# Kernel optimization log

Measured on AMD Instinct MI355X. Metric: run time of the kernel, lower is better.

## Reference

```python
import jax, jax.numpy as jnp
import numpy as np

# Dimensions
T = 1024      # tokens
D = 1024      # d_model
DFF = 1024    # expert intermediate dim
R = 64        # tucker rank (r_in == r_out)
G = 8         # n_group
E = 32        # experts_per_group
NEXP = G * E  # 256 routed experts
K = 8         # top-k


def setup_inputs() -> dict:
    key = jax.random.key(0)
    ks = jax.random.split(key, 12)
    s = 0.02
    return {
        "x": jax.random.normal(ks[0], (T, D), jnp.float32),
        "Wg": jax.random.normal(ks[1], (D, NEXP), jnp.float32) * s,
        "uin_gate": jax.random.normal(ks[2], (G, D, R), jnp.float32) * s,
        "core_gate": jax.random.normal(ks[3], (G, E, R, R), jnp.float32) * s,
        "uout_gate": jax.random.normal(ks[4], (G, R, DFF), jnp.float32) * s,
        "uin_up": jax.random.normal(ks[5], (G, D, R), jnp.float32) * s,
        "core_up": jax.random.normal(ks[6], (G, E, R, R), jnp.float32) * s,
        "uout_up": jax.random.normal(ks[7], (G, R, DFF), jnp.float32) * s,
        "uin_down": jax.random.normal(ks[8], (G, DFF, R), jnp.float32) * s,
        "core_down": jax.random.normal(ks[9], (G, E, R, R), jnp.float32) * s,
        "uout_down": jax.random.normal(ks[10], (G, R, D), jnp.float32) * s,
    }


def _moe_forward(x, Wg, uin_gate, core_gate, uout_gate,
                 uin_up, core_up, uout_up,
                 uin_down, core_down, uout_down):
    Tn, d = x.shape
    # Router: top-k over 256 experts, softmax over the k logits (fp32 as in torch)
    logits = x @ Wg                                   # [T, NEXP]
    w, sel = jax.lax.top_k(logits, K)                 # [T, K]
    w = jax.nn.softmax(w.astype(jnp.float32), axis=-1).astype(x.dtype)

    e = sel.reshape(-1)                               # [F] global expert id
    g = e // E                                        # [F] group id
    tok = jnp.repeat(jnp.arange(Tn), K)               # [F] source token id
    mask = (g[:, None] == jnp.arange(G)[None, :]).astype(x.dtype)  # [F, G]

    def gather_in(uin):
        # project tokens with every group's u_in once, then gather per pair
        pre = jnp.einsum('td,gdr->gtr', x, uin)       # [G, T, R]
        return pre[g, tok]                            # [F, R]

    def core_apply(xin, core):
        # per-pair Tucker core slice bmm: x.unsqueeze(1) @ core[rel_idx]
        slices = core.reshape(G * E, R, R)[e]         # [F, R, R] gather
        return jnp.einsum('fr,fro->fo', xin, slices)  # [F, R]

    def group_out(h, U):
        # per-pair group-specific projection: h[f] @ U[g_f]
        out = jnp.zeros((h.shape[0], U.shape[-1]), h.dtype)
        for gi in range(G):  # fixed small loop over 8 groups
            out = out + (h * mask[:, gi:gi + 1]) @ U[gi]
        return out

    gate_h = group_out(core_apply(gather_in(uin_gate), core_gate), uout_gate)  # [F, DFF]
    up_h = group_out(core_apply(gather_in(uin_up), core_up), uout_up)          # [F, DFF]
    act = jax.nn.silu(gate_h) * up_h                                           # SwiGLU
    xin_d = group_out(act, uin_down)                                           # [F, R]
    out_f = group_out(core_apply(xin_d, core_down), uout_down)                 # [F, D]
    out_f = out_f * w.reshape(-1)[:, None]
    # scatter-add expert outputs back to tokens
    return jax.ops.segment_sum(out_f, tok, num_segments=Tn)


def reference(x, Wg, uin_gate, core_gate, uout_gate,
              uin_up, core_up, uout_up,
              uin_down, core_down, uout_down):
    return _moe_forward(x, Wg, uin_gate, core_gate, uout_gate,
                        uin_up, core_up, uout_up,
                        uin_down, core_down, uout_down)
```

## Files before the change

### kernel.cpp

```cpp
#include <hip/hip_runtime.h>
#include <hip/hip_bf16.h>
#include <math.h>


#define T_ 1024
#define D_ 1024
#define DFF_ 1024
#define R_ 64
#define G_ 8
#define E_ 32
#define NEXP_ 256
#define K_ 8
#define F_ 8192
#define PKZ_ 2
#define DKZ_ 4
#define LP_ 72

typedef short bf16x8 __attribute__((ext_vector_type(8)));
typedef float f32x4 __attribute__((ext_vector_type(4)));

__device__ __forceinline__ unsigned short f2bf(float f) {
  unsigned int u = __float_as_uint(f);
  u += 0x7fffu + ((u >> 16) & 1u);
  return (unsigned short)(u >> 16);
}

__device__ __forceinline__ void stage_tile(short* dst, const unsigned short* src,
                                           int gp, int tid) {
  for (int idx = tid; idx < 512; idx += 256) {
    int r = idx >> 3, c8 = (idx & 7) << 3;
    *(uint4*)&dst[r * LP_ + c8] = *(const uint4*)&src[(size_t)r * gp + c8];
  }
}

__device__ __forceinline__ void stage_tile_guard(short* dst, const unsigned short* src,
                                                 int gp, int rows_valid, int tid) {
  for (int idx = tid; idx < 512; idx += 256) {
    int r = idx >> 3, c8 = (idx & 7) << 3;
    uint4 v = make_uint4(0u, 0u, 0u, 0u);
    if (r < rows_valid) v = *(const uint4*)&src[(size_t)r * gp + c8];
    *(uint4*)&dst[r * LP_ + c8] = v;
  }
}

__device__ __forceinline__ void stage_tile_f32(short* dst, const float* src,
                                               int gp, int tid) {
  for (int idx = tid; idx < 512; idx += 256) {
    int r = idx >> 3, c8 = (idx & 7) << 3;
    const float* s = &src[(size_t)r * gp + c8];
    float4 v0 = *(const float4*)s;
    float4 v1 = *(const float4*)(s + 4);
    uint4 u;
    u.x = ((unsigned)f2bf(v0.y) << 16) | f2bf(v0.x);
    u.y = ((unsigned)f2bf(v0.w) << 16) | f2bf(v0.z);
    u.z = ((unsigned)f2bf(v1.y) << 16) | f2bf(v1.x);
    u.w = ((unsigned)f2bf(v1.w) << 16) | f2bf(v1.z);
    *(uint4*)&dst[r * LP_ + c8] = u;
  }
}

__device__ __forceinline__ void mma_strip(const short* As, const short* Bs,
                                          int ms, int lane, f32x4* acc) {
  int lm = lane & 15;
  int lk = (lane >> 4) << 3;
#pragma unroll
  for (int kc = 0; kc < 64; kc += 32) {
    bf16x8 a = *(const bf16x8*)&As[(ms + lm) * LP_ + kc + lk];
#pragma unroll
    for (int nt = 0; nt < 4; ++nt) {
      bf16x8 b = *(const bf16x8*)&Bs[(nt * 16 + lm) * LP_ + kc + lk];
      acc[nt] = __builtin_amdgcn_mfma_f32_16x16x32_bf16(a, b, acc[nt], 0, 0, 0);
    }
  }
}

__global__ __launch_bounds__(256) void k_prep(
    const float* __restrict__ x,
    const float* __restrict__ s0, const float* __restrict__ s1,
    const float* __restrict__ s2, const float* __restrict__ s3,
    const float* __restrict__ s4, const float* __restrict__ s5,
    unsigned short* __restrict__ xb,
    unsigned short* __restrict__ d0, unsigned short* __restrict__ d1,
    unsigned short* __restrict__ d2, unsigned short* __restrict__ d3,
    unsigned short* __restrict__ d4, unsigned short* __restrict__ d5,
    int* __restrict__ cnt, int* __restrict__ tickets, float* __restrict__ Yf) {
  __shared__ float shbuf[64 * 65];
  int b = blockIdx.x;
  int id = b >> 7, rem = b & 127, g = rem >> 4, tile = rem & 15;
  if (id == 6) {
    size_t base = ((size_t)g * 16 + tile) * 8192;
    for (int i = threadIdx.x; i < 2048; i += 256) {
      size_t idx = base + (size_t)i * 4;
      float4 v = *(const float4*)&x[idx];
      xb[idx + 0] = f2bf(v.x);
      xb[idx + 1] = f2bf(v.y);
      xb[idx + 2] = f2bf(v.z);
      xb[idx + 3] = f2bf(v.w);
    }
    size_t ybase = ((size_t)g * 16 + tile) * 4096;
    float4 z4 = make_float4(0.f, 0.f, 0.f, 0.f);
    for (int i = threadIdx.x; i < 1024; i += 256)
      *(float4*)&Yf[ybase + (size_t)i * 4] = z4;
    if (g == 0 && tile == 0) {
      cnt[threadIdx.x] = 0;
      if (threadIdx.x == 0) tickets[0] = 0;
    }
    return;
  }
  const float* src = id == 0 ? s0 : id == 1 ? s1 : id == 2 ? s2 : id == 3 ? s3 : id == 4 ? s4 : s5;
  unsigned short* dst = id == 0 ? d0 : id == 1 ? d1 : id == 2 ? d2 : id == 3 ? d3 : id == 4 ? d4 : d5;
  if (id < 3) {
    int r0 = tile * 64;
    for (int idx = threadIdx.x; idx < 4096; idx += 256) {
      int r = idx >> 6, c = idx & 63;
      shbuf[r * 65 + c] = src[((size_t)g * 1024 + r0 + r) * 64 + c];
    }
    __syncthreads();
    for (int idx = threadIdx.x; idx < 4096; idx += 256) {
      int c = idx >> 6, r = idx & 63;
      dst[((size_t)g * 64 + c) * 1024 + r0 + r] = f2bf(shbuf[r * 65 + c]);
    }
  } else {
    int c0 = tile * 64;
    for (int idx = threadIdx.x; idx < 4096; idx += 256) {
      int r = idx >> 6, c = idx & 63;
      shbuf[r * 65 + c] = src[((size_t)g * 64 + r) * 1024 + c0 + c];
    }
    __syncthreads();
    if (id == 5) {
      for (int idx = threadIdx.x; idx < 4096; idx += 256) {
        int c = idx >> 6, r = idx & 63;
        dst[(size_t)(c0 + c) * 512 + g * 64 + r] = f2bf(shbuf[r * 65 + c]);
      }
    } else {
      for (int idx = threadIdx.x; idx < 4096; idx += 256) {
        int c = idx >> 6, r = idx & 63;
        dst[((size_t)g * 1024 + c0 + c) * 64 + r] = f2bf(shbuf[r * 65 + c]);
      }
    }
  }
}

__global__ __launch_bounds__(256) void k_pre_router(
    const float* __restrict__ x, const float* __restrict__ Wg,
    const unsigned short* __restrict__ xb,
    const unsigned short* __restrict__ uinT_g, const unsigned short* __restrict__ uinT_u,
    float* __restrict__ Pgp, float* __restrict__ Pup,
    float* __restrict__ wsm, int* __restrict__ bucket, int* __restrict__ cnt,
    int* __restrict__ tickets, int* __restrict__ off) {
  __shared__ float smf[8192];
  __shared__ int lastfl;
  int b = blockIdx.x;
  int tid = threadIdx.x;
  if (b >= 128) {
    int b2 = b - 128;
    int tile = b2 & 15, g = (b2 >> 4) & 7, zz = b2 >> 7;
    int gu = zz >> 1, kz = zz & 1;
    const unsigned short* U = gu ? uinT_u : uinT_g;
    float* P = gu ? Pup : Pgp;
    int t0 = tile * 64;
    short* As = (short*)smf;
    short* Bs = (short*)smf + 64 * LP_;
    int lane = tid & 63, ms = (tid >> 6) * 16;
    f32x4 acc[4] = {};
    int dlo = kz * (D_ / PKZ_);
    for (int dc = dlo; dc < dlo + D_ / PKZ_; dc += 64) {
      stage_tile(As, xb + (size_t)t0 * D_ + dc, D_, tid);
      stage_tile(Bs, U + (size_t)g * 64 * 1024 + dc, 1024, tid);
      __syncthreads();
      mma_strip(As, Bs, ms, lane, acc);
      __syncthreads();
    }
    int lm = lane & 15, lq = (lane >> 4) * 4;
#pragma unroll
    for (int nt = 0; nt < 4; ++nt)
#pragma unroll
      for (int r = 0; r < 4; ++r)
        P[((size_t)(kz * G_ + g) * T_ + t0 + ms + lq + r) * R_ + nt * 16 + lm] = acc[nt][r];
    return;
  }
  int t0 = b * 8;
  for (int i = tid; i < 2048; i += 256) {
    int j = i >> 8, d4 = (i & 255) << 2;
    *(float4*)&smf[j * 1024 + d4] = *(const float4*)&x[(size_t)(t0 + j) * D_ + d4];
  }
  __syncthreads();
  int e = tid;
  float a[8] = {};
#pragma unroll 2
  for (int d2 = 0; d2 < 1024; d2 += 4) {
    float w0 = Wg[(size_t)(d2 + 0) * NEXP_ + e];
    float w1 = Wg[(size_t)(d2 + 1) * NEXP_ + e];
    float w2 = Wg[(size_t)(d2 + 2) * NEXP_ + e];
    float w3 = Wg[(size_t)(d2 + 3) * NEXP_ + e];
#pragma unroll
    for (int j = 0; j < 8; ++j) {
      float4 xv = *(const float4*)&smf[j * 1024 + d2];
      float aj = a[j];
      aj = fmaf(xv.x, w0, aj);
      aj = fmaf(xv.y, w1, aj);
      aj = fmaf(xv.z, w2, aj);
      aj = fmaf(xv.w, w3, aj);
      a[j] = aj;
    }
  }
  __syncthreads();
  float* lg = smf;
#pragma unroll
  for (int j = 0; j < 8; ++j) lg[j * 256 + e] = a[j];
  __syncthreads();
  int wave = tid >> 6, lane = tid & 63;
  for (int kk = 0; kk < 2; ++kk) {
    int j = wave * 2 + kk;
    int t = t0 + j;
    float v[4];
    int idx[4];
#pragma unroll
    for (int j2 = 0; j2 < 4; ++j2) {
      idx[j2] = lane + 64 * j2;
      v[j2] = lg[j * 256 + idx[j2]];
    }
    float topv[K_];
    int topi[K_];
#pragma unroll
    for (int k = 0; k < K_; ++k) {
      float bv = v[0];
      int bi = idx[0];
#pragma unroll
      for (int j2 = 1; j2 < 4; ++j2)
        if (v[j2] > bv || (v[j2] == bv && idx[j2] < bi)) { bv = v[j2]; bi = idx[j2]; }
#pragma unroll
      for (int o2 = 32; o2 > 0; o2 >>= 1) {
        float ov = __shfl_xor(bv, o2);
        int oi = __shfl_xor(bi, o2);
        if (ov > bv || (ov == bv && oi < bi)) { bv = ov; bi = oi; }
      }
      topv[k] = bv;
      topi[k] = bi;
#pragma unroll
      for (int j2 = 0; j2 < 4; ++j2)
        if (idx[j2] == bi) v[j2] = -INFINITY;
    }
    float m = topv[0];
    float ev[K_];
    float s = 0.f;
#pragma unroll
    for (int k = 0; k < K_; ++k) { ev[k] = expf(topv[k] - m); s += ev[k]; }
    float inv = 1.f / s;
    if (lane < K_) {
      wsm[t * K_ + lane] = ev[lane] * inv;
      int r1 = atomicAdd(&cnt[topi[lane]], 1);
      bucket[topi[lane] * 1024 + r1] = t * K_ + lane;
    }
  }
  __threadfence();
  __syncthreads();
  if (tid == 0) lastfl = (atomicAdd(&tickets[0], 1) == 127) ? 1 : 0;
  __syncthreads();
  if (lastfl) {
    int* s = (int*)smf;
    int i = tid;
    int c0 = atomicAdd(&cnt[i], 0);
    s[i] = c0;
    __syncthreads();
    for (int d = 1; d < NEXP_; d <<= 1) {
      int vv = (i >= d) ? s[i - d] : 0;
      __syncthreads();
      s[i] += vv;
      __syncthreads();
    }
    off[i + 1] = s[i];
    if (i == 0) off[0] = 0;
  }
}

__global__ __launch_bounds__(256) void k_core_gu(const float* __restrict__ Pgp,
                                                 const float* __restrict__ Pup,
                                                 const float* __restrict__ core_g,
                                                 const float* __restrict__ core_u,
                                                 const int* __restrict__ bucket,
                                                 const int* __restrict__ off,
                                                 unsigned short* __restrict__ xgb,
                                                 unsigned short* __restrict__ xub) {
  int e = blockIdx.x >> 1, half = blockIdx.x & 1;
  int g = e >> 5;
  __shared__ float cg[4096], cu[4096];
  __shared__ float rg[4][64], ru[4][64];
  int tid = threadIdx.x;
  for (int i = tid; i < 1024; i += 256) {
    *(float4*)&cg[i * 4] = *(const float4*)&core_g[(size_t)e * 4096 + (size_t)i * 4];
    *(float4*)&cu[i * 4] = *(const float4*)&core_u[(size_t)e * 4096 + (size_t)i * 4];
  }
  int p0 = off[e], n = off[e + 1] - p0;
  int hn = (n + 1) >> 1;
  int i0 = half * hn;
  int i1 = i0 + hn; if (i1 > n) i1 = n;
  int pl = tid >> 6, o = tid & 63;
  __syncthreads();
  for (int ib = i0; ib < i1; ib += 4) {
    int i = ib + pl;
    bool valid = i < i1;
    int p = p0 + i;
    float sg = 0.f, su = 0.f;
    if (valid) {
      int t = bucket[e * 1024 + i] >> 3;
#pragma unroll
      for (int kz = 0; kz < PKZ_; ++kz) {
        sg += Pgp[((size_t)(kz * G_ + g) * T_ + t) * R_ + o];
        su += Pup[((size_t)(kz * G_ + g) * T_ + t) * R_ + o];
      }
    }
    __syncthreads();
    rg[pl][o] = sg;
    ru[pl][o] = su;
    __syncthreads();
    if (valid) {
      float ag = 0.f, au = 0.f;
#pragma unroll 8
      for (int r = 0; r < R_; ++r) {
        ag = fmaf(rg[pl][r], cg[r * R_ + o], ag);
        au = fmaf(ru[pl][r], cu[r * R_ + o], au);
      }
      xgb[(size_t)p * R_ + o] = f2bf(ag);
      xub[(size_t)p * R_ + o] = f2bf(au);
    }
  }
}

__global__ __launch_bounds__(256) void k_fused_ad(const unsigned short* __restrict__ xgb,
                                                  const unsigned short* __restrict__ xub,
                                                  const unsigned short* __restrict__ uoutT_g,
                                                  const unsigned short* __restrict__ uoutT_u,
                                                  const unsigned short* __restrict__ uinT_d,
                                                  const int* __restrict__ off,
                                                  float* __restrict__ xdp) {
  int g = blockIdx.y;
  int kz = blockIdx.z;
  int p0 = off[g * E_];
  int pend = off[g * E_ + E_];
  int ntiles = (pend - p0 + 63) >> 6;
  __shared__ short Ag[64 * LP_], Au[64 * LP_];
  __shared__ short Bg[64 * LP_], Bu[64 * LP_], Bd[64 * LP_];
  __shared__ short Pt[64 * LP_];
  int tid = threadIdx.x, lane = tid & 63, ms = (tid >> 6) * 16;
  int lm = lane & 15, lq = (lane >> 4) * 4;
  for (int tile = blockIdx.x; tile < ntiles; tile += gridDim.x) {
    int pbase = p0 + tile * 64;
    int rv = pend - pbase; if (rv > 64) rv = 64;
    stage_tile_guard(Ag, xgb + (size_t)pbase * R_, R_, rv, tid);
    stage_tile_guard(Au, xub + (size_t)pbase * R_, R_, rv, tid);
    f32x4 accd[4] = {};
#pragma unroll
    for (int c4 = 0; c4 < 4; ++c4) {
      int cc = kz * (DFF_ / DKZ_) + c4 * 64;
      stage_tile(Bg, uoutT_g + ((size_t)g * DFF_ + cc) * R_, R_, tid);
      stage_tile(Bu, uoutT_u + ((size_t)g * DFF_ + cc) * R_, R_, tid);
      stage_tile(Bd, uinT_d + (size_t)g * 64 * 1024 + cc, 1024, tid);
      __syncthreads();
      f32x4 accg[4] = {}, accu[4] = {};
      mma_strip(Ag, Bg, ms, lane, accg);
      mma_strip(Au, Bu, ms, lane, accu);
#pragma unroll
      for (int nt = 0; nt < 4; ++nt)
#pragma unroll
        for (int r = 0; r < 4; ++r) {
          float gv = accg[nt][r];
          float av = gv / (1.f + expf(-gv)) * accu[nt][r];
          Pt[(ms + lq + r) * LP_ + nt * 16 + lm] = (short)f2bf(av);
        }
      mma_strip(Pt, Bd, ms, lane, accd);
      __syncthreads();
    }
#pragma unroll
    for (int nt = 0; nt < 4; ++nt)
#pragma unroll
      for (int r = 0; r < 4; ++r) {
        int p = pbase + ms + lq + r;
        if (p < pend) xdp[((size_t)kz * F_ + p) * R_ + nt * 16 + lm] = accd[nt][r];
      }
    __syncthreads();
  }
}

__global__ __launch_bounds__(256) void k_down_core(const float* __restrict__ xdp,
                                                   const float* __restrict__ core_d,
                                                   const int* __restrict__ bucket,
                                                   const float* __restrict__ wsm,
                                                   const int* __restrict__ off,
                                                   float* __restrict__ Yf) {
  int e = blockIdx.x >> 1, half = blockIdx.x & 1;
  int g = e >> 5;
  __shared__ float cd[4096];
  __shared__ float xs[4][64];
  int tid = threadIdx.x;
  for (int i = tid; i < 1024; i += 256)
    *(float4*)&cd[i * 4] = *(const float4*)&core_d[(size_t)e * 4096 + (size_t)i * 4];
  int p0 = off[e], n = off[e + 1] - p0;
  int hn = (n + 1) >> 1;
  int i0 = half * hn;
  int i1 = i0 + hn; if (i1 > n) i1 = n;
  int pl = tid >> 6, o = tid & 63;
  __syncthreads();
  for (int ib = i0; ib < i1; ib += 4) {
    int i = ib + pl;
    bool valid = i < i1;
    int p = p0 + i;
    int f = valid ? bucket[e * 1024 + i] : 0;
    float s = 0.f;
    if (valid) {
#pragma unroll
      for (int kz = 0; kz < DKZ_; ++kz) s += xdp[((size_t)kz * F_ + p) * R_ + o];
    }
    __syncthreads();
    xs[pl][o] = s;
    __syncthreads();
    if (valid) {
      float a = 0.f;
#pragma unroll 8
      for (int r = 0; r < R_; ++r) a = fmaf(xs[pl][r], cd[r * R_ + o], a);
      atomicAdd(&Yf[(size_t)(f >> 3) * 512 + g * 64 + o], wsm[f] * a);
    }
  }
}

__global__ __launch_bounds__(256) void k_fin(const float* __restrict__ Yf,
                                             const unsigned short* __restrict__ Uod2T,
                                             float* __restrict__ out) {
  int t0 = blockIdx.x * 64;
  int d0 = blockIdx.y * 64;
  __shared__ short As[64 * LP_], Bs[64 * LP_];
  __shared__ float Os[64 * 68];
  int tid = threadIdx.x, lane = tid & 63, ms = (tid >> 6) * 16;
  int lm = lane & 15, lq = (lane >> 4) * 4;
  f32x4 acc[4] = {};
  for (int kc = 0; kc < 512; kc += 64) {
    stage_tile_f32(As, Yf + (size_t)t0 * 512 + kc, 512, tid);
    stage_tile(Bs, Uod2T + (size_t)d0 * 512 + kc, 512, tid);
    __syncthreads();
    mma_strip(As, Bs, ms, lane, acc);
    __syncthreads();
  }
#pragma unroll
  for (int nt = 0; nt < 4; ++nt)
#pragma unroll
    for (int r = 0; r < 4; ++r)
      Os[(ms + lq + r) * 68 + nt * 16 + lm] = acc[nt][r];
  __syncthreads();
  for (int idx = tid; idx < 1024; idx += 256) {
    int r = idx >> 4, c4 = (idx & 15) << 2;
    *(float4*)&out[(size_t)(t0 + r) * D_ + d0 + c4] = *(const float4*)&Os[r * 68 + c4];
  }
}

extern "C" void kernel_launch(void* const* d_in, const int* in_sizes, int n_in,
                              void* d_out, int out_size, void* d_ws, size_t ws_size,
                              hipStream_t stream) {
  const float* x = (const float*)d_in[0];
  const float* Wg = (const float*)d_in[1];
  const float* uin_gate = (const float*)d_in[2];
  const float* core_gate = (const float*)d_in[3];
  const float* uout_gate = (const float*)d_in[4];
  const float* uin_up = (const float*)d_in[5];
  const float* core_up = (const float*)d_in[6];
  const float* uout_up = (const float*)d_in[7];
  const float* uin_down = (const float*)d_in[8];
  const float* core_down = (const float*)d_in[9];
  const float* uout_down = (const float*)d_in[10];
  float* out = (float*)d_out;

  char* ws = (char*)d_ws;
  size_t o = 0;
  auto alloc = [&](size_t bytes) { size_t r = o; o = (o + bytes + 255) & ~(size_t)255; return r; };
  size_t o_wsm = alloc(F_ * 4);
  size_t o_bucket = alloc((size_t)NEXP_ * 1024 * 4);
  size_t o_cnt = alloc(NEXP_ * 4);
  size_t o_tickets = alloc(256);
  size_t o_off = alloc((NEXP_ + 1) * 4);
  size_t o_xb = alloc((size_t)T_ * D_ * 2);
  size_t o_uinT_g = alloc((size_t)G_ * 64 * 1024 * 2);
  size_t o_uinT_u = alloc((size_t)G_ * 64 * 1024 * 2);
  size_t o_uinT_d = alloc((size_t)G_ * 64 * 1024 * 2);
  size_t o_uoutT_g = alloc((size_t)G_ * 1024 * 64 * 2);
  size_t o_uoutT_u = alloc((size_t)G_ * 1024 * 64 * 2);
  size_t o_Uod2T = alloc((size_t)D_ * 512 * 2);
  size_t o_xgb = alloc((size_t)F_ * R_ * 2);
  size_t o_xub = alloc((size_t)F_ * R_ * 2);
  size_t o_Y = alloc((size_t)T_ * 512 * 4);
  size_t o_pgp = alloc((size_t)PKZ_ * G_ * T_ * R_ * 4);
  size_t o_pup = alloc((size_t)PKZ_ * G_ * T_ * R_ * 4);
  size_t o_xdp = alloc((size_t)DKZ_ * F_ * R_ * 4);
  (void)ws_size;

  float* wsm = (float*)(ws + o_wsm);
  int* bucket = (int*)(ws + o_bucket);
  int* cnt = (int*)(ws + o_cnt);
  int* tickets = (int*)(ws + o_tickets);
  int* off = (int*)(ws + o_off);
  unsigned short* xb = (unsigned short*)(ws + o_xb);
  unsigned short* uinT_g = (unsigned short*)(ws + o_uinT_g);
  unsigned short* uinT_u = (unsigned short*)(ws + o_uinT_u);
  unsigned short* uinT_d = (unsigned short*)(ws + o_uinT_d);
  unsigned short* uoutT_g = (unsigned short*)(ws + o_uoutT_g);
  unsigned short* uoutT_u = (unsigned short*)(ws + o_uoutT_u);
  unsigned short* Uod2T = (unsigned short*)(ws + o_Uod2T);
  unsigned short* xgb = (unsigned short*)(ws + o_xgb);
  unsigned short* xub = (unsigned short*)(ws + o_xub);
  float* Yf = (float*)(ws + o_Y);
  float* pgp = (float*)(ws + o_pgp);
  float* pup = (float*)(ws + o_pup);
  float* xdp = (float*)(ws + o_xdp);

  k_prep<<<896, 256, 0, stream>>>(x, uin_gate, uin_up, uin_down,
                                  uout_gate, uout_up, uout_down, xb,
                                  uinT_g, uinT_u, uinT_d,
                                  uoutT_g, uoutT_u, Uod2T, cnt, tickets, Yf);
  k_pre_router<<<640, 256, 0, stream>>>(x, Wg, xb, uinT_g, uinT_u,
                                        pgp, pup, wsm, bucket, cnt, tickets, off);
  k_core_gu<<<NEXP_ * 2, 256, 0, stream>>>(pgp, pup, core_gate, core_up, bucket, off, xgb, xub);
  k_fused_ad<<<dim3(16, G_, DKZ_), 256, 0, stream>>>(xgb, xub, uoutT_g, uoutT_u, uinT_d, off, xdp);
  k_down_core<<<NEXP_ * 2, 256, 0, stream>>>(xdp, core_down, bucket, wsm, off, Yf);
  k_fin<<<dim3(16, 16), 256, 0, stream>>>(Yf, Uod2T, out);
}
```

Before: 239.6 us.

## Split router matmul across waves by d-slices with 4 tokens per block

The router blocks now handle 4 tokens each instead of 8, doubling the router block count to 256. Each wave accumulates a 256-wide slice of the d dimension for all 256 experts, and the partial sums are reduced through shared memory before top-k. The aim is more parallelism and a shorter serial dot-product loop in the router part of the fused launch. The cost is that each block re-reads all of Wg for only 4 tokens, doubling total Wg traffic, and adds a shared-memory reduction step.

```diff
diff --git a/kernel.cpp b/kernel.cpp
--- a/kernel.cpp
+++ b/kernel.cpp
@@ -152,8 +152,8 @@
   __shared__ int lastfl;
   int b = blockIdx.x;
   int tid = threadIdx.x;
-  if (b >= 128) {
-    int b2 = b - 128;
+  if (b >= 256) {
+    int b2 = b - 256;
     int tile = b2 & 15, g = (b2 >> 4) & 7, zz = b2 >> 7;
     int gu = zz >> 1, kz = zz & 1;
     const unsigned short* U = gu ? uinT_u : uinT_g;
@@ -179,46 +179,80 @@
         P[((size_t)(kz * G_ + g) * T_ + t0 + ms + lq + r) * R_ + nt * 16 + lm] = acc[nt][r];
     return;
   }
-  int t0 = b * 8;
-  for (int i = tid; i < 2048; i += 256) {
+  int t0 = b * 4;
+  float* xs = smf;
+  float* part = smf + 4096;
+  for (int i = tid; i < 1024; i += 256) {
     int j = i >> 8, d4 = (i & 255) << 2;
-    *(float4*)&smf[j * 1024 + d4] = *(const float4*)&x[(size_t)(t0 + j) * D_ + d4];
-  }
-  __syncthreads();
-  int e = tid;
-  float a[8] = {};
+    *(float4*)&xs[j * 1024 + d4] = *(const float4*)&x[(size_t)(t0 + j) * D_ + d4];
+  }
+  __syncthreads();
+  int wv = tid >> 6, lane = tid & 63;
+  int dbase = wv * 256;
+  float a00 = 0.f, a01 = 0.f, a02 = 0.f, a03 = 0.f;
+  float a10 = 0.f, a11 = 0.f, a12 = 0.f, a13 = 0.f;
+  float a20 = 0.f, a21 = 0.f, a22 = 0.f, a23 = 0.f;
+  float a30 = 0.f, a31 = 0.f, a32 = 0.f, a33 = 0.f;
 #pragma unroll 2
-  for (int d2 = 0; d2 < 1024; d2 += 4) {
-    float w0 = Wg[(size_t)(d2 + 0) * NEXP_ + e];
-    float w1 = Wg[(size_t)(d2 + 1) * NEXP_ + e];
-    float w2 = Wg[(size_t)(d2 + 2) * NEXP_ + e];
-    float w3 = Wg[(size_t)(d2 + 3) * NEXP_ + e];
-#pragma unroll
-    for (int j = 0; j < 8; ++j) {
-      float4 xv = *(const float4*)&smf[j * 1024 + d2];
-      float aj = a[j];
-      aj = fmaf(xv.x, w0, aj);
-      aj = fmaf(xv.y, w1, aj);
-      aj = fmaf(xv.z, w2, aj);
-      aj = fmaf(xv.w, w3, aj);
-      a[j] = aj;
-    }
-  }
-  __syncthreads();
-  float* lg = smf;
-#pragma unroll
-  for (int j = 0; j < 8; ++j) lg[j * 256 + e] = a[j];
-  __syncthreads();
-  int wave = tid >> 6, lane = tid & 63;
-  for (int kk = 0; kk < 2; ++kk) {
-    int j = wave * 2 + kk;
-    int t = t0 + j;
+  for (int d2 = 0; d2 < 256; d2 += 4) {
+    int d = dbase + d2;
+    float4 xv0 = *(const float4*)&xs[0 * 1024 + d];
+    float4 xv1 = *(const float4*)&xs[1 * 1024 + d];
+    float4 xv2 = *(const float4*)&xs[2 * 1024 + d];
+    float4 xv3 = *(const float4*)&xs[3 * 1024 + d];
+#pragma unroll
+    for (int j = 0; j < 4; ++j) {
+      int e = lane + 64 * j;
+      float w0 = Wg[(size_t)(d + 0) * NEXP_ + e];
+      float w1 = Wg[(size_t)(d + 1) * NEXP_ + e];
+      float w2 = Wg[(size_t)(d + 2) * NEXP_ + e];
+      float w3 = Wg[(size_t)(d + 3) * NEXP_ + e];
+      float t00 = j == 0 ? a00 : j == 1 ? a10 : j == 2 ? a20 : a30;
+      float t01 = j == 0 ? a01 : j == 1 ? a11 : j == 2 ? a21 : a31;
+      float t02 = j == 0 ? a02 : j == 1 ? a12 : j == 2 ? a22 : a32;
+      float t03 = j == 0 ? a03 : j == 1 ? a13 : j == 2 ? a23 : a33;
+      t00 = fmaf(xv0.x, w0, t00); t00 = fmaf(xv0.y, w1, t00);
+      t00 = fmaf(xv0.z, w2, t00); t00 = fmaf(xv0.w, w3, t00);
+      t01 = fmaf(xv1.x, w0, t01); t01 = fmaf(xv1.y, w1, t01);
+      t01 = fmaf(xv1.z, w2, t01); t01 = fmaf(xv1.w, w3, t01);
+      t02 = fmaf(xv2.x, w0, t02); t02 = fmaf(xv2.y, w1, t02);
+      t02 = fmaf(xv2.z, w2, t02); t02 = fmaf(xv2.w, w3, t02);
+      t03 = fmaf(xv3.x, w0, t03); t03 = fmaf(xv3.y, w1, t03);
+      t03 = fmaf(xv3.z, w2, t03); t03 = fmaf(xv3.w, w3, t03);
+      if (j == 0) { a00 = t00; a01 = t01; a02 = t02; a03 = t03; }
+      else if (j == 1) { a10 = t00; a11 = t01; a12 = t02; a13 = t03; }
+      else if (j == 2) { a20 = t00; a21 = t01; a22 = t02; a23 = t03; }
+      else { a30 = t00; a31 = t01; a32 = t02; a33 = t03; }
+    }
+  }
+  part[(wv * 4 + 0) * 256 + lane + 0]   = a00;
+  part[(wv * 4 + 1) * 256 + lane + 0]   = a01;
+  part[(wv * 4 + 2) * 256 + lane + 0]   = a02;
+  part[(wv * 4 + 3) * 256 + lane + 0]   = a03;
+  part[(wv * 4 + 0) * 256 + lane + 64]  = a10;
+  part[(wv * 4 + 1) * 256 + lane + 64]  = a11;
+  part[(wv * 4 + 2) * 256 + lane + 64]  = a12;
+  part[(wv * 4 + 3) * 256 + lane + 64]  = a13;
+  part[(wv * 4 + 0) * 256 + lane + 128] = a20;
+  part[(wv * 4 + 1) * 256 + lane + 128] = a21;
+  part[(wv * 4 + 2) * 256 + lane + 128] = a22;
+  part[(wv * 4 + 3) * 256 + lane + 128] = a23;
+  part[(wv * 4 + 0) * 256 + lane + 192] = a30;
+  part[(wv * 4 + 1) * 256 + lane + 192] = a31;
+  part[(wv * 4 + 2) * 256 + lane + 192] = a32;
+  part[(wv * 4 + 3) * 256 + lane + 192] = a33;
+  __syncthreads();
+  {
+    int tt = wv;
+    int t = t0 + tt;
     float v[4];
     int idx[4];
 #pragma unroll
     for (int j2 = 0; j2 < 4; ++j2) {
-      idx[j2] = lane + 64 * j2;
-      v[j2] = lg[j * 256 + idx[j2]];
+      int e = lane + 64 * j2;
+      idx[j2] = e;
+      v[j2] = part[(0 * 4 + tt) * 256 + e] + part[(1 * 4 + tt) * 256 + e]
+            + part[(2 * 4 + tt) * 256 + e] + part[(3 * 4 + tt) * 256 + e];
     }
     float topv[K_];
     int topi[K_];
@@ -255,7 +289,7 @@
   }
   __threadfence();
   __syncthreads();
-  if (tid == 0) lastfl = (atomicAdd(&tickets[0], 1) == 127) ? 1 : 0;
+  if (tid == 0) lastfl = (atomicAdd(&tickets[0], 1) == 255) ? 1 : 0;
   __syncthreads();
   if (lastfl) {
     int* s = (int*)smf;
@@ -514,7 +548,7 @@
                                   uout_gate, uout_up, uout_down, xb,
                                   uinT_g, uinT_u, uinT_d,
                                   uoutT_g, uoutT_u, Uod2T, cnt, tickets, Yf);
-  k_pre_router<<<640, 256, 0, stream>>>(x, Wg, xb, uinT_g, uinT_u,
+  k_pre_router<<<768, 256, 0, stream>>>(x, Wg, xb, uinT_g, uinT_u,
                                         pgp, pup, wsm, bucket, cnt, tickets, off);
   k_core_gu<<<NEXP_ * 2, 256, 0, stream>>>(pgp, pup, core_gate, core_up, bucket, off, xgb, xub);
   k_fused_ad<<<dim3(16, G_, DKZ_), 256, 0, stream>>>(xgb, xub, uoutT_g, uoutT_u, uinT_d, off, xdp);
```

Result: faster. 218.8 us (-8.7%).
